# Optimization experiments

Measured on AMD Instinct MI355X. Metric: run time of the kernel, lower is better.

Reference implementation:

```python
import jax, jax.numpy as jnp
import numpy as np

EPS_SLOPE = 1e-4
EPS_AVG = 1e-8
MIN_AVG = 1e-6
EPS_SCALE = 1e-3


def _slopes_yk(xk, delta_raw):
    # xk: [D, K] sorted knot x-positions; delta_raw: [D, K-1]
    seg_dx = xk[:, 1:] - xk[:, :-1]                      # [D, K-1]
    slopes = jax.nn.softplus(delta_raw) + EPS_SLOPE       # [D, K-1]
    avg = (slopes * seg_dx).sum(1, keepdims=True) / (seg_dx.sum(1, keepdims=True) + EPS_AVG)
    avg = jnp.maximum(avg, MIN_AVG)
    slopes = slopes / avg
    yk = jnp.concatenate(
        [jnp.zeros((xk.shape[0], 1), dtype=xk.dtype), jnp.cumsum(slopes * seg_dx, axis=1)],
        axis=1,
    )                                                     # [D, K]
    return slopes, yk


def setup_inputs() -> dict:
    key = jax.random.key(0)
    k1, k2, k3, k4, k5 = jax.random.split(key, 5)
    N, D, K = 1_000_000, 64, 32
    x = jax.random.normal(k1, (N, D), dtype=jnp.float32)
    # sorted knots per dim, spanning roughly the data range
    xk = jnp.sort(jax.random.normal(k2, (D, K), dtype=jnp.float32) * 2.0, axis=1)
    delta_raw = jax.random.normal(k3, (D, K - 1), dtype=jnp.float32) * 0.1
    scale_raw = jax.random.normal(k4, (D,), dtype=jnp.float32) * 0.1
    shift = jax.random.normal(k5, (D,), dtype=jnp.float32) * 0.1
    return {"x": x, "xk": xk, "delta_raw": delta_raw, "scale_raw": scale_raw, "shift": shift}


def reference(x, xk, delta_raw, scale_raw, shift):
    # x: [N, D]; xk: [D, K]
    D, K = xk.shape
    slopes, yk = _slopes_yk(xk, delta_raw)
    xT = x.T                                              # [D, N]
    # per-dim binary search (torch.searchsorted default == side='left')
    idx = jax.vmap(lambda knots, vals: jnp.searchsorted(knots, vals))(xk, xT)
    i0 = jnp.clip(idx, 1, K - 1) - 1                      # [D, N]
    x0 = jnp.take_along_axis(xk, i0, axis=1)              # [D, N]
    y0 = jnp.take_along_axis(yk, i0, axis=1)
    m = jnp.take_along_axis(slopes, i0, axis=1)
    y = (y0 + m * (xT - x0)).T                            # [N, D]
    scale = jax.nn.softplus(scale_raw) + EPS_SCALE
    return y * scale + shift
```

## Files before the change

### kernel.cpp

```cpp
#include <hip/hip_runtime.h>
#include <math.h>

#define D 64
#define KNOTS 32
#define NSEG 31
#define G 512
#define TPAD 516
#define SPAD 33

typedef float f4v __attribute__((ext_vector_type(4)));

__device__ __forceinline__ float softplus_f(float v) {
  return fmaxf(v, 0.f) + log1pf(expf(-fabsf(v)));
}

__global__ __launch_bounds__(1024, 8) void pwl_fused(
    const float* __restrict__ x, const float* __restrict__ xk,
    const float* __restrict__ delta_raw, const float* __restrict__ scale_raw,
    const float* __restrict__ shift, float* __restrict__ out, int nrows) {
  __shared__ float kL[KNOTS * D];
  __shared__ float sA[D * SPAD];
  __shared__ float sB[D * SPAD];
  __shared__ unsigned char tab[D * TPAD];
  __shared__ float invS[D], nloS[D];

  const int tid = threadIdx.x;

  for (int i = tid; i < D * KNOTS; i += blockDim.x) {
    int d = i >> 5, j = i & 31;
    int sd = (d >> 2) | ((d & 3) << 4);
    kL[j * D + sd] = xk[i];
  }
  __syncthreads();

  if (tid < D) {
    const int sd = tid;
    const int d = ((sd & 15) << 2) | (sd >> 4);
    float num = 0.f, den = 0.f;
    for (int s = 0; s < NSEG; ++s) {
      float sp = softplus_f(delta_raw[d * NSEG + s]) + 1e-4f;
      float dx = kL[(s + 1) * D + sd] - kL[s * D + sd];
      num += sp * dx;
      den += dx;
    }
    float avg = fmaxf(num / (den + 1e-8f), 1e-6f);
    float scale = softplus_f(scale_raw[d]) + 1e-3f;
    float sh = shift[d];
    float y = 0.f;
    for (int s = 0; s < NSEG; ++s) {
      float sp = softplus_f(delta_raw[d * NSEG + s]) + 1e-4f;
      float m = sp / avg;
      float k0 = kL[s * D + sd];
      sA[sd * SPAD + s] = m * scale;
      sB[sd * SPAD + s] = (y - m * k0) * scale + sh;
      y += m * (kL[(s + 1) * D + sd] - k0);
    }
    float lo = kL[1 * D + sd];
    float hi = kL[(KNOTS - 1) * D + sd];
    float inv = (float)G / (hi - lo);
    invS[sd] = inv;
    nloS[sd] = -lo * inv;
  }
  __syncthreads();

  for (int p = tid; p < G * D; p += blockDim.x) {
    const int sd = p & 63;
    const int c = p >> 6;
    const float inv = invS[sd], nlo = nloS[sd];
    int b = 0;
#pragma unroll
    for (int half = 16; half > 0; half >>= 1) {
      float kv = kL[(b + half) * D + sd];
      float cf = fminf(fmaxf(fmaf(kv, inv, nlo), 0.f), (float)(G - 1));
      b += ((int)cf < c) ? half : 0;
    }
    tab[sd * TPAD + c] = (unsigned char)min(b, 30);
  }
  __syncthreads();

  const int lane = tid & 63;
  const int q = lane & 15;
  const int sd0 = q, sd1 = q + 16, sd2 = q + 32, sd3 = q + 48;
  const float inv0 = invS[sd0], nlo0 = nloS[sd0];
  const float inv1 = invS[sd1], nlo1 = nloS[sd1];
  const float inv2 = invS[sd2], nlo2 = nloS[sd2];
  const float inv3 = invS[sd3], nlo3 = nloS[sd3];

  const f4v* __restrict__ x4 = (const f4v*)x;
  f4v* __restrict__ o4 = (f4v*)out;

  auto evalquad = [&](f4v xv) -> f4v {
    float cf0 = fminf(fmaxf(fmaf(xv.x, inv0, nlo0), 0.f), (float)(G - 1));
    float cf1 = fminf(fmaxf(fmaf(xv.y, inv1, nlo1), 0.f), (float)(G - 1));
    float cf2 = fminf(fmaxf(fmaf(xv.z, inv2, nlo2), 0.f), (float)(G - 1));
    float cf3 = fminf(fmaxf(fmaf(xv.w, inv3, nlo3), 0.f), (float)(G - 1));
    int i0 = tab[sd0 * TPAD + (int)cf0];
    int i1 = tab[sd1 * TPAD + (int)cf1];
    int i2 = tab[sd2 * TPAD + (int)cf2];
    int i3 = tab[sd3 * TPAD + (int)cf3];
    f4v r;
    r.x = fmaf(sA[sd0 * SPAD + i0], xv.x, sB[sd0 * SPAD + i0]);
    r.y = fmaf(sA[sd1 * SPAD + i1], xv.y, sB[sd1 * SPAD + i1]);
    r.z = fmaf(sA[sd2 * SPAD + i2], xv.z, sB[sd2 * SPAD + i2]);
    r.w = fmaf(sA[sd3 * SPAD + i3], xv.w, sB[sd3 * SPAD + i3]);
    return r;
  };

  const int gwave = (int)(blockIdx.x * blockDim.x + tid) >> 6;
  const int nwave = (int)(gridDim.x * blockDim.x) >> 6;
  const int ngroups = nrows >> 4;
  const int chunk = (ngroups + nwave - 1) / nwave;
  int g = gwave * chunk;
  const int gend = min(g + chunk, ngroups);

  f4v a0, a1, a2, a3;
  f4v b0, b1, b2, b3;

#define LOADG(p, gg)                                      \
  {                                                       \
    const int base_ = (gg) * 256 + lane;                  \
    p##0 = x4[base_];        p##1 = x4[base_ + 64];       \
    p##2 = x4[base_ + 128];  p##3 = x4[base_ + 192];      \
  }

#define PROCG(p, gg)                                                        \
  {                                                                         \
    const int base_ = (gg) * 256 + lane;                                    \
    f4v r_;                                                                 \
    r_ = evalquad(p##0); __builtin_nontemporal_store(r_, &o4[base_]);       \
    r_ = evalquad(p##1); __builtin_nontemporal_store(r_, &o4[base_ + 64]);  \
    r_ = evalquad(p##2); __builtin_nontemporal_store(r_, &o4[base_ + 128]); \
    r_ = evalquad(p##3); __builtin_nontemporal_store(r_, &o4[base_ + 192]); \
  }

  if (g < gend) {
    LOADG(a, g);
    while (true) {
      const int gn = g + 1;
      if (gn < gend) {
        LOADG(b, gn);
        PROCG(a, g);
        const int gnn = gn + 1;
        if (gnn < gend) {
          LOADG(a, gnn);
          PROCG(b, gn);
          g = gnn;
        } else {
          PROCG(b, gn);
          break;
        }
      } else {
        PROCG(a, g);
        break;
      }
    }
  }
#undef LOADG
#undef PROCG

  const int tr0 = ngroups << 4;
  for (int r = tr0 + gwave; r < nrows; r += nwave) {
    if (lane < 16) {
      const int bi = r * 16 + q;
      f4v xv = x4[bi];
      f4v rv = evalquad(xv);
      __builtin_nontemporal_store(rv, &o4[bi]);
    }
  }
}

extern "C" void kernel_launch(void* const* d_in, const int* in_sizes, int n_in,
                              void* d_out, int out_size, void* d_ws, size_t ws_size,
                              hipStream_t stream) {
  const float* x = (const float*)d_in[0];
  const float* xk = (const float*)d_in[1];
  const float* delta_raw = (const float*)d_in[2];
  const float* scale_raw = (const float*)d_in[3];
  const float* shift = (const float*)d_in[4];
  float* out = (float*)d_out;

  const int nrows = in_sizes[0] / D;
  const int block = 1024;
  const int grid = 512;
  pwl_fused<<<grid, block, 0, stream>>>(x, xk, delta_raw, scale_raw, shift,
                                        out, nrows);
}
```

Measured before the change: 113.8 us.

## Deepen software pipeline to four groups in flight with smaller 8-row groups

Shrinks the per-wave row group from 16 to 8 rows and replaces the two-buffer double-buffered loop with a four-buffer rotating pipeline. Three groups are prefetched ahead of the one being processed, with load indices clamped to the last group so the loop needs no branchy tail. The aim is to keep more independent global loads in flight per wave and hide memory latency on this bandwidth-bound streaming kernel. The register footprint for prefetched data stays the same, but the clamping issues redundant reloads of the last group near the end of each wave's chunk.

Measured after the change: 114.9 us. About the same (+1.0%).

```diff
diff --git a/kernel.cpp b/kernel.cpp
--- a/kernel.cpp
+++ b/kernel.cpp
@@ -108,57 +108,49 @@
 
   const int gwave = (int)(blockIdx.x * blockDim.x + tid) >> 6;
   const int nwave = (int)(gridDim.x * blockDim.x) >> 6;
-  const int ngroups = nrows >> 4;
+  const int ngroups = nrows >> 3;
   const int chunk = (ngroups + nwave - 1) / nwave;
   int g = gwave * chunk;
   const int gend = min(g + chunk, ngroups);
 
-  f4v a0, a1, a2, a3;
-  f4v b0, b1, b2, b3;
+  f4v a0, a1, b0, b1, c0, c1, d0, d1;
 
-#define LOADG(p, gg)                                      \
-  {                                                       \
-    const int base_ = (gg) * 256 + lane;                  \
-    p##0 = x4[base_];        p##1 = x4[base_ + 64];       \
-    p##2 = x4[base_ + 128];  p##3 = x4[base_ + 192];      \
+#define LOADG(p, gg)                            \
+  {                                             \
+    const int base_ = (gg) * 128 + lane;        \
+    p##0 = x4[base_];                           \
+    p##1 = x4[base_ + 64];                      \
   }
 
-#define PROCG(p, gg)                                                        \
-  {                                                                         \
-    const int base_ = (gg) * 256 + lane;                                    \
-    f4v r_;                                                                 \
-    r_ = evalquad(p##0); __builtin_nontemporal_store(r_, &o4[base_]);       \
-    r_ = evalquad(p##1); __builtin_nontemporal_store(r_, &o4[base_ + 64]);  \
-    r_ = evalquad(p##2); __builtin_nontemporal_store(r_, &o4[base_ + 128]); \
-    r_ = evalquad(p##3); __builtin_nontemporal_store(r_, &o4[base_ + 192]); \
+#define PROCG(p, gg)                                                       \
+  {                                                                        \
+    const int base_ = (gg) * 128 + lane;                                   \
+    f4v r_;                                                                \
+    r_ = evalquad(p##0); __builtin_nontemporal_store(r_, &o4[base_]);      \
+    r_ = evalquad(p##1); __builtin_nontemporal_store(r_, &o4[base_ + 64]); \
   }
 
   if (g < gend) {
-    LOADG(a, g);
+    const int glast = gend - 1;
+    int gl = g;
+    LOADG(a, gl); gl = min(gl + 1, glast);
+    LOADG(b, gl); gl = min(gl + 1, glast);
+    LOADG(c, gl); gl = min(gl + 1, glast);
     while (true) {
-      const int gn = g + 1;
-      if (gn < gend) {
-        LOADG(b, gn);
-        PROCG(a, g);
-        const int gnn = gn + 1;
-        if (gnn < gend) {
-          LOADG(a, gnn);
-          PROCG(b, gn);
-          g = gnn;
-        } else {
-          PROCG(b, gn);
-          break;
-        }
-      } else {
-        PROCG(a, g);
-        break;
-      }
+      LOADG(d, gl); gl = min(gl + 1, glast);
+      PROCG(a, g); if (++g == gend) break;
+      LOADG(a, gl); gl = min(gl + 1, glast);
+      PROCG(b, g); if (++g == gend) break;
+      LOADG(b, gl); gl = min(gl + 1, glast);
+      PROCG(c, g); if (++g == gend) break;
+      LOADG(c, gl); gl = min(gl + 1, glast);
+      PROCG(d, g); if (++g == gend) break;
     }
   }
 #undef LOADG
 #undef PROCG
 
-  const int tr0 = ngroups << 4;
+  const int tr0 = ngroups << 3;
   for (int r = tr0 + gwave; r < nrows; r += nwave) {
     if (lane < 16) {
       const int bi = r * 16 + q;
```
